# Kernel tuning notes

Hardware: AMD Instinct MI355X
Metric: run time of the kernel (lower is better)

## Reference

```python
import jax, jax.numpy as jnp
import numpy as np

N, E = 50000, 800000
DIN, DOUT = 256, 128
DH = 2 * DOUT  # hidden width of conv1


def setup_inputs() -> dict:
    key = jax.random.key(0)
    ks = jax.random.split(key, 9)
    x = jax.random.normal(ks[0], (N, DIN), dtype=jnp.float32)
    edge_index = jax.random.randint(ks[1], (2, E), 0, N, dtype=jnp.int64)
    edge_weight = jax.random.uniform(ks[2], (E,), dtype=jnp.float32)
    s1 = 1.0 / np.sqrt(DIN)
    s2 = 1.0 / np.sqrt(DH)
    W1 = jax.random.uniform(ks[3], (DIN, DH), minval=-s1, maxval=s1, dtype=jnp.float32)
    b1 = jnp.zeros((DH,), jnp.float32)
    Wmu = jax.random.uniform(ks[4], (DH, DOUT), minval=-s2, maxval=s2, dtype=jnp.float32)
    bmu = jnp.zeros((DOUT,), jnp.float32)
    Wls = jax.random.uniform(ks[5], (DH, DOUT), minval=-s2, maxval=s2, dtype=jnp.float32)
    bls = jnp.zeros((DOUT,), jnp.float32)
    return {"x": x, "edge_index": edge_index, "edge_weight": edge_weight,
            "W1": W1, "b1": b1, "Wmu": Wmu, "bmu": bmu, "Wls": Wls, "bls": bls}


def _gcn_layer(x, row, col, norm, W, b, n):
    # GCNConv: linear transform, then normalized scatter-add aggregation, then bias
    h = x @ W                                   # [N, Dout]
    msg = h[row] * norm[:, None]                # gather source feats, scale per-edge
    agg = jax.ops.segment_sum(msg, col, num_segments=n)  # scatter-add to targets
    return agg + b


def reference(x, edge_index, edge_weight, W1, b1, Wmu, bmu, Wls, bls):
    n = x.shape[0]
    row, col = edge_index[0], edge_index[1]
    # add self loops with weight 1 (PyG gcn_norm default, fill_value=1)
    loop = jnp.arange(n)
    row_f = jnp.concatenate([row, loop])
    col_f = jnp.concatenate([col, loop])
    ew = jnp.concatenate([edge_weight, jnp.ones((n,), x.dtype)])
    # symmetric normalization: deg computed over destination index
    deg = jax.ops.segment_sum(ew, col_f, num_segments=n)
    dinv = jnp.where(deg > 0, jax.lax.rsqrt(deg), 0.0)
    norm = dinv[row_f] * ew * dinv[col_f]       # cached=True -> same norm each layer
    h = jax.nn.relu(_gcn_layer(x, row_f, col_f, norm, W1, b1, n))
    mu = _gcn_layer(h, row_f, col_f, norm, Wmu, bmu, n)
    logstd = _gcn_layer(h, row_f, col_f, norm, Wls, bls, n)
    return mu, logstd
```

## Files before the change

### kernel.cpp

```cpp
#include <hip/hip_runtime.h>

#define THREADS 256

typedef __attribute__((ext_vector_type(8))) short bf16x8;
typedef __attribute__((ext_vector_type(4))) float f32x4;

#define CNT_SHIFT 20
#define DEG_SCALE 8192.0f
#define DEG_MASK  ((1u << CNT_SHIFT) - 1)

__device__ inline float bf2f(unsigned short u) {
    union { unsigned int i; float f; } v; v.i = ((unsigned int)u) << 16; return v.f;
}
__device__ inline unsigned short f2bf(float f) {
    union { float f; unsigned int i; } v; v.f = f;
    unsigned int i = v.i;
    i += 0x7fff + ((i >> 16) & 1);
    return (unsigned short)(i >> 16);
}

__global__ void k_count(const int* __restrict__ dst, const float* __restrict__ ew,
                        unsigned int* __restrict__ packed,
                        int* __restrict__ rank, int E) {
    int e = blockIdx.x * THREADS + threadIdx.x;
    if (e >= E) return;
    int c = dst[e];
    unsigned int v = (1u << CNT_SHIFT) | (unsigned int)(ew[e] * DEG_SCALE + 0.5f);
    unsigned int old = atomicAdd(&packed[c], v);
    rank[e] = (int)(old >> CNT_SHIFT);
}

__global__ void k_scan_part(const unsigned int* __restrict__ packed,
                            int* __restrict__ counts, float* __restrict__ dinv,
                            int* __restrict__ offsets, int* __restrict__ blocksum, int n) {
    __shared__ int s[THREADS];
    int i = blockIdx.x * THREADS + threadIdx.x;
    unsigned int p = (i < n) ? packed[i] : 0u;
    int v = (int)(p >> CNT_SHIFT);
    if (i < n) {
        counts[i] = v;
        float d = 1.0f + (float)(p & DEG_MASK) * (1.0f / DEG_SCALE);
        dinv[i] = rsqrtf(d);
    }
    s[threadIdx.x] = v;
    __syncthreads();
    for (int d = 1; d < THREADS; d <<= 1) {
        int t = (threadIdx.x >= d) ? s[threadIdx.x - d] : 0;
        __syncthreads();
        s[threadIdx.x] += t;
        __syncthreads();
    }
    if (i < n) offsets[i] = s[threadIdx.x] - v;
    if (threadIdx.x == THREADS - 1) blocksum[blockIdx.x] = s[THREADS - 1];
}

__global__ void k_scan_block(int* __restrict__ blocksum, int nb) {
    __shared__ int s[THREADS];
    int v = (threadIdx.x < nb) ? blocksum[threadIdx.x] : 0;
    s[threadIdx.x] = v;
    __syncthreads();
    for (int d = 1; d < THREADS; d <<= 1) {
        int t = (threadIdx.x >= d) ? s[threadIdx.x - d] : 0;
        __syncthreads();
        s[threadIdx.x] += t;
        __syncthreads();
    }
    if (threadIdx.x < nb) blocksum[threadIdx.x] = s[threadIdx.x] - v;
}

__global__ void k_scan_add(int* __restrict__ offsets, const int* __restrict__ blocksum, int n) {
    int i = blockIdx.x * THREADS + threadIdx.x;
    if (i >= n) return;
    offsets[i] += blocksum[blockIdx.x];
}

__global__ void k_fill(const int* __restrict__ ei, const float* __restrict__ ew,
                       const float* __restrict__ dinv, const int* __restrict__ offsets,
                       const int* __restrict__ rank, int2* __restrict__ epack, int E) {
    int e = blockIdx.x * THREADS + threadIdx.x;
    if (e >= E) return;
    int r = ei[e];
    int c = ei[E + e];
    int pos = offsets[c] + rank[e];
    int2 m; m.x = r; m.y = __float_as_int(dinv[r] * ew[e] * dinv[c]);
    epack[pos] = m;
}

__global__ void k_cvt_w(const float* __restrict__ W1, const float* __restrict__ Wmu,
                        const float* __restrict__ Wls, const float* __restrict__ bmu,
                        const float* __restrict__ bls,
                        ushort* __restrict__ W1t, ushort* __restrict__ Wct,
                        float* __restrict__ bcat, unsigned int* __restrict__ packed,
                        int n) {
    int nb = blockIdx.x, k = threadIdx.x;
    int gi = nb * THREADS + k;
    if (gi < n) packed[gi] = 0u;
    if (nb < 256) {
        W1t[k * 256 + nb] = f2bf(W1[nb * 256 + k]);
    } else if (nb < 512) {
        int r = nb - 256;
        float v = (k < 128) ? Wmu[r * 128 + k] : Wls[r * 128 + (k - 128)];
        Wct[k * 256 + r] = f2bf(v);
    } else {
        bcat[k] = (k < 128) ? bmu[k] : bls[k - 128];
    }
}

template<int MODE>
__global__ void k_agg(const ushort4* __restrict__ fb,
                      const int* __restrict__ eoff, const int* __restrict__ ecnt,
                      const int2* __restrict__ epack, const float* __restrict__ dinv,
                      const float* __restrict__ bias, void* __restrict__ out, int n) {
    int wave = threadIdx.x >> 6, lane = threadIdx.x & 63;
    int node = blockIdx.x * 4 + wave;
    if (node >= n) return;
    float ds = dinv[node]; ds *= ds;
    ushort4 v = fb[(size_t)node * 64 + lane];
    float ax = ds * bf2f(v.x), ay = ds * bf2f(v.y),
          az = ds * bf2f(v.z), aw = ds * bf2f(v.w);
    int e = eoff[node], cnt = ecnt[node];
    while (cnt > 0) {
        int take = cnt < 64 ? cnt : 64;
        int2 meta = make_int2(0, 0);
        if (lane < take) {
            long long m = __builtin_nontemporal_load((const long long*)&epack[e + lane]);
            meta.x = (int)m; meta.y = (int)(m >> 32);
        }
        for (int j = 0; j < take; j += 8) {
            int s0 = __builtin_amdgcn_readlane(meta.x, j + 0);
            int s1 = __builtin_amdgcn_readlane(meta.x, j + 1);
            int s2 = __builtin_amdgcn_readlane(meta.x, j + 2);
            int s3 = __builtin_amdgcn_readlane(meta.x, j + 3);
            int s4 = __builtin_amdgcn_readlane(meta.x, j + 4);
            int s5 = __builtin_amdgcn_readlane(meta.x, j + 5);
            int s6 = __builtin_amdgcn_readlane(meta.x, j + 6);
            int s7 = __builtin_amdgcn_readlane(meta.x, j + 7);
            float w0 = __int_as_float(__builtin_amdgcn_readlane(meta.y, j + 0));
            float w1 = __int_as_float(__builtin_amdgcn_readlane(meta.y, j + 1));
            float w2 = __int_as_float(__builtin_amdgcn_readlane(meta.y, j + 2));
            float w3 = __int_as_float(__builtin_amdgcn_readlane(meta.y, j + 3));
            float w4 = __int_as_float(__builtin_amdgcn_readlane(meta.y, j + 4));
            float w5 = __int_as_float(__builtin_amdgcn_readlane(meta.y, j + 5));
            float w6 = __int_as_float(__builtin_amdgcn_readlane(meta.y, j + 6));
            float w7 = __int_as_float(__builtin_amdgcn_readlane(meta.y, j + 7));
            ushort4 u0 = fb[(size_t)s0 * 64 + lane];
            ushort4 u1 = fb[(size_t)s1 * 64 + lane];
            ushort4 u2 = fb[(size_t)s2 * 64 + lane];
            ushort4 u3 = fb[(size_t)s3 * 64 + lane];
            ushort4 u4 = fb[(size_t)s4 * 64 + lane];
            ushort4 u5 = fb[(size_t)s5 * 64 + lane];
            ushort4 u6 = fb[(size_t)s6 * 64 + lane];
            ushort4 u7 = fb[(size_t)s7 * 64 + lane];
            ax += w0 * bf2f(u0.x) + w1 * bf2f(u1.x) + w2 * bf2f(u2.x) + w3 * bf2f(u3.x);
            ay += w0 * bf2f(u0.y) + w1 * bf2f(u1.y) + w2 * bf2f(u2.y) + w3 * bf2f(u3.y);
            az += w0 * bf2f(u0.z) + w1 * bf2f(u1.z) + w2 * bf2f(u2.z) + w3 * bf2f(u3.z);
            aw += w0 * bf2f(u0.w) + w1 * bf2f(u1.w) + w2 * bf2f(u2.w) + w3 * bf2f(u3.w);
            ax += w4 * bf2f(u4.x) + w5 * bf2f(u5.x) + w6 * bf2f(u6.x) + w7 * bf2f(u7.x);
            ay += w4 * bf2f(u4.y) + w5 * bf2f(u5.y) + w6 * bf2f(u6.y) + w7 * bf2f(u7.y);
            az += w4 * bf2f(u4.z) + w5 * bf2f(u5.z) + w6 * bf2f(u6.z) + w7 * bf2f(u7.z);
            aw += w4 * bf2f(u4.w) + w5 * bf2f(u5.w) + w6 * bf2f(u6.w) + w7 * bf2f(u7.w);
        }
        e += take; cnt -= take;
    }
    float4 b = ((const float4*)bias)[lane];
    ax += b.x; ay += b.y; az += b.z; aw += b.w;
    if (MODE == 0) {
        unsigned long long o =
            (unsigned long long)f2bf(fmaxf(ax, 0.f)) |
            ((unsigned long long)f2bf(fmaxf(ay, 0.f)) << 16) |
            ((unsigned long long)f2bf(fmaxf(az, 0.f)) << 32) |
            ((unsigned long long)f2bf(fmaxf(aw, 0.f)) << 48);
        __builtin_nontemporal_store(o, (unsigned long long*)out + (size_t)node * 64 + lane);
    } else {
        f32x4 o; o[0] = ax; o[1] = ay; o[2] = az; o[3] = aw;
        f32x4* mu = (f32x4*)out;
        f32x4* ls = mu + (size_t)n * 32;
        if (lane < 32) __builtin_nontemporal_store(o, &mu[(size_t)node * 32 + lane]);
        else           __builtin_nontemporal_store(o, &ls[(size_t)node * 32 + (lane - 32)]);
    }
}

#define LDT 40
template<int AF32>
__global__ __launch_bounds__(256) void k_gemm(const void* __restrict__ Ain,
        const ushort* __restrict__ Bt, ushort* __restrict__ C, int M) {
    __shared__ ushort As[128 * LDT];
    __shared__ ushort Bs[128 * LDT];
    const float*  Af = (const float*)Ain;
    const ushort* Ab = (const ushort*)Ain;
    int tid = threadIdx.x;
    int lane = tid & 63, wave = tid >> 6;
    int row0 = blockIdx.y * 128, col0 = blockIdx.x * 128;
    int mw = (wave >> 1) * 64, nw = (wave & 1) * 64;
    int lr = lane & 15, lq = lane >> 4;
    f32x4 acc[4][4] = {};
    for (int k0 = 0; k0 < 256; k0 += 32) {
        #pragma unroll
        for (int i = 0; i < 2; i++) {
            int c = tid + i * 256;
            int r = c >> 2, q = c & 3;
            int gr = row0 + r;
            int4 av = make_int4(0, 0, 0, 0);
            if (gr < M) {
                if (AF32) {
                    const float* p = Af + (size_t)gr * 256 + k0 + q * 8;
                    float4 lo = *(const float4*)p;
                    float4 hi = *(const float4*)(p + 4);
                    ushort* u = (ushort*)&av;
                    u[0] = f2bf(lo.x); u[1] = f2bf(lo.y);
                    u[2] = f2bf(lo.z); u[3] = f2bf(lo.w);
                    u[4] = f2bf(hi.x); u[5] = f2bf(hi.y);
                    u[6] = f2bf(hi.z); u[7] = f2bf(hi.w);
                } else {
                    av = *(const int4*)(Ab + (size_t)gr * 256 + k0 + q * 8);
                }
            }
            *(int4*)(&As[r * LDT + q * 8]) = av;
            int4 bv = *(const int4*)(Bt + (size_t)(col0 + r) * 256 + k0 + q * 8);
            *(int4*)(&Bs[r * LDT + q * 8]) = bv;
        }
        __syncthreads();
        bf16x8 af[4], bfr[4];
        #pragma unroll
        for (int mi = 0; mi < 4; mi++)
            af[mi] = *(const bf16x8*)(&As[(mw + mi * 16 + lr) * LDT + lq * 8]);
        #pragma unroll
        for (int ni = 0; ni < 4; ni++)
            bfr[ni] = *(const bf16x8*)(&Bs[(nw + ni * 16 + lr) * LDT + lq * 8]);
        #pragma unroll
        for (int mi = 0; mi < 4; mi++)
            #pragma unroll
            for (int ni = 0; ni < 4; ni++)
                acc[mi][ni] = __builtin_amdgcn_mfma_f32_16x16x32_bf16(
                    af[mi], bfr[ni], acc[mi][ni], 0, 0, 0);
        __syncthreads();
    }
    #pragma unroll
    for (int mi = 0; mi < 4; mi++)
        #pragma unroll
        for (int ni = 0; ni < 4; ni++)
            #pragma unroll
            for (int r = 0; r < 4; r++) {
                int grow = row0 + mw + mi * 16 + lq * 4 + r;
                int gcol = col0 + nw + ni * 16 + lr;
                if (grow < M) C[(size_t)grow * 256 + gcol] = f2bf(acc[mi][ni][r]);
            }
}

extern "C" void kernel_launch(void* const* d_in, const int* in_sizes, int n_in,
                              void* d_out, int out_size, void* d_ws, size_t ws_size,
                              hipStream_t stream) {
    const float* x   = (const float*)d_in[0];
    const int*   ei  = (const int*)d_in[1];
    const float* ew  = (const float*)d_in[2];
    const float* W1  = (const float*)d_in[3];
    const float* b1  = (const float*)d_in[4];
    const float* Wmu = (const float*)d_in[5];
    const float* bmu = (const float*)d_in[6];
    const float* Wls = (const float*)d_in[7];
    const float* bls = (const float*)d_in[8];

    const int DIN = 256;
    const int N = in_sizes[0] / DIN;
    const int E = in_sizes[2];

    unsigned int* packed = (unsigned int*)d_ws;
    int*   counts   = (int*)(packed + N);
    int*   offsets  = counts + N;
    float* dinv     = (float*)(offsets + N);
    int*   blocksum = (int*)(dinv + N);
    int*   rank     = blocksum + 256;
    int2*  epack    = (int2*)(rank + E);
    ushort* xw      = (ushort*)(epack + E);
    ushort* hb      = xw + (size_t)N * 256;
    ushort* hw      = hb + (size_t)N * 256;
    ushort* W1t     = hw + (size_t)N * 256;
    ushort* Wct     = W1t + 256 * 256;
    float*  bcat    = (float*)(Wct + 256 * 256);

    int gN = (N + THREADS - 1) / THREADS;
    int gE = (E + THREADS - 1) / THREADS;

    k_cvt_w<<<513, THREADS, 0, stream>>>(W1, Wmu, Wls, bmu, bls, W1t, Wct, bcat,
                                         packed, N);
    k_count<<<gE, THREADS, 0, stream>>>(ei + E, ew, packed, rank, E);

    k_scan_part<<<gN, THREADS, 0, stream>>>(packed, counts, dinv, offsets, blocksum, N);
    k_scan_block<<<1, THREADS, 0, stream>>>(blocksum, gN);
    k_scan_add<<<gN, THREADS, 0, stream>>>(offsets, blocksum, N);

    k_fill<<<gE, THREADS, 0, stream>>>(ei, ew, dinv, offsets, rank, epack, E);

    int gAgg = (N + 3) / 4;
    dim3 ggrid(2, (N + 127) / 128);

    k_gemm<1><<<ggrid, 256, 0, stream>>>(x, W1t, xw, N);
    k_agg<0><<<gAgg, THREADS, 0, stream>>>((const ushort4*)xw, offsets, counts,
                                           epack, dinv, b1, hb, N);

    k_gemm<0><<<ggrid, 256, 0, stream>>>(hb, Wct, hw, N);
    k_agg<1><<<gAgg, THREADS, 0, stream>>>((const ushort4*)hw, offsets, counts,
                                           epack, dinv, bcat, d_out, N);
}
```

Before: 358.0 us.

## Widen GEMM tile to full output width, fold scan-add into consumers, nontemporal loads

The GEMM now uses 512-thread blocks, each covering all 256 output columns for a 128-row tile. The A tile (including the fp32-to-bf16 conversion of x) is therefore loaded and converted once per row block instead of twice. The separate scan-add kernel is removed, and the block prefix sums are added on the fly in k_fill and k_agg, saving one launch and one pass over the offsets array. Streaming loads and stores in the count, fill and GEMM kernels are marked nontemporal to reduce cache pollution. In exchange, the larger GEMM tile doubles LDS use for B and may lower occupancy.

```diff
diff --git a/kernel.cpp b/kernel.cpp
--- a/kernel.cpp
+++ b/kernel.cpp
@@ -4,6 +4,7 @@
 
 typedef __attribute__((ext_vector_type(8))) short bf16x8;
 typedef __attribute__((ext_vector_type(4))) float f32x4;
+typedef __attribute__((ext_vector_type(4))) int i32x4;
 
 #define CNT_SHIFT 20
 #define DEG_SCALE 8192.0f
@@ -24,10 +25,11 @@
                         int* __restrict__ rank, int E) {
     int e = blockIdx.x * THREADS + threadIdx.x;
     if (e >= E) return;
-    int c = dst[e];
-    unsigned int v = (1u << CNT_SHIFT) | (unsigned int)(ew[e] * DEG_SCALE + 0.5f);
+    int c = __builtin_nontemporal_load(dst + e);
+    float w = __builtin_nontemporal_load(ew + e);
+    unsigned int v = (1u << CNT_SHIFT) | (unsigned int)(w * DEG_SCALE + 0.5f);
     unsigned int old = atomicAdd(&packed[c], v);
-    rank[e] = (int)(old >> CNT_SHIFT);
+    __builtin_nontemporal_store((int)(old >> CNT_SHIFT), rank + e);
 }
 
 __global__ void k_scan_part(const unsigned int* __restrict__ packed,
@@ -68,22 +70,20 @@
     if (threadIdx.x < nb) blocksum[threadIdx.x] = s[threadIdx.x] - v;
 }
 
-__global__ void k_scan_add(int* __restrict__ offsets, const int* __restrict__ blocksum, int n) {
-    int i = blockIdx.x * THREADS + threadIdx.x;
-    if (i >= n) return;
-    offsets[i] += blocksum[blockIdx.x];
-}
-
 __global__ void k_fill(const int* __restrict__ ei, const float* __restrict__ ew,
                        const float* __restrict__ dinv, const int* __restrict__ offsets,
+                       const int* __restrict__ bsum,
                        const int* __restrict__ rank, int2* __restrict__ epack, int E) {
     int e = blockIdx.x * THREADS + threadIdx.x;
     if (e >= E) return;
-    int r = ei[e];
-    int c = ei[E + e];
-    int pos = offsets[c] + rank[e];
-    int2 m; m.x = r; m.y = __float_as_int(dinv[r] * ew[e] * dinv[c]);
-    epack[pos] = m;
+    int r = __builtin_nontemporal_load(ei + e);
+    int c = __builtin_nontemporal_load(ei + E + e);
+    float w = __builtin_nontemporal_load(ew + e);
+    int rk = __builtin_nontemporal_load(rank + e);
+    int pos = offsets[c] + bsum[c >> 8] + rk;
+    long long m = (long long)r |
+        ((long long)__float_as_int(dinv[r] * w * dinv[c]) << 32);
+    __builtin_nontemporal_store(m, (long long*)&epack[pos]);
 }
 
 __global__ void k_cvt_w(const float* __restrict__ W1, const float* __restrict__ Wmu,
@@ -109,6 +109,7 @@
 template<int MODE>
 __global__ void k_agg(const ushort4* __restrict__ fb,
                       const int* __restrict__ eoff, const int* __restrict__ ecnt,
+                      const int* __restrict__ bsum,
                       const int2* __restrict__ epack, const float* __restrict__ dinv,
                       const float* __restrict__ bias, void* __restrict__ out, int n) {
     int wave = threadIdx.x >> 6, lane = threadIdx.x & 63;
@@ -118,7 +119,7 @@
     ushort4 v = fb[(size_t)node * 64 + lane];
     float ax = ds * bf2f(v.x), ay = ds * bf2f(v.y),
           az = ds * bf2f(v.z), aw = ds * bf2f(v.w);
-    int e = eoff[node], cnt = ecnt[node];
+    int e = eoff[node] + bsum[node >> 8], cnt = ecnt[node];
     while (cnt > 0) {
         int take = cnt < 64 ? cnt : 64;
         int2 meta = make_int2(0, 0);
@@ -182,42 +183,46 @@
 
 #define LDT 40
 template<int AF32>
-__global__ __launch_bounds__(256) void k_gemm(const void* __restrict__ Ain,
+__global__ __launch_bounds__(512) void k_gemm(const void* __restrict__ Ain,
         const ushort* __restrict__ Bt, ushort* __restrict__ C, int M) {
     __shared__ ushort As[128 * LDT];
-    __shared__ ushort Bs[128 * LDT];
+    __shared__ ushort Bs[256 * LDT];
     const float*  Af = (const float*)Ain;
     const ushort* Ab = (const ushort*)Ain;
     int tid = threadIdx.x;
     int lane = tid & 63, wave = tid >> 6;
-    int row0 = blockIdx.y * 128, col0 = blockIdx.x * 128;
-    int mw = (wave >> 1) * 64, nw = (wave & 1) * 64;
+    int row0 = blockIdx.x * 128;
+    int mw = (wave >> 2) * 64, nw = (wave & 3) * 64;
     int lr = lane & 15, lq = lane >> 4;
     f32x4 acc[4][4] = {};
     for (int k0 = 0; k0 < 256; k0 += 32) {
-        #pragma unroll
-        for (int i = 0; i < 2; i++) {
-            int c = tid + i * 256;
-            int r = c >> 2, q = c & 3;
+        {
+            int r = tid >> 2, q = tid & 3;
             int gr = row0 + r;
-            int4 av = make_int4(0, 0, 0, 0);
+            i32x4 av = {0, 0, 0, 0};
             if (gr < M) {
                 if (AF32) {
                     const float* p = Af + (size_t)gr * 256 + k0 + q * 8;
-                    float4 lo = *(const float4*)p;
-                    float4 hi = *(const float4*)(p + 4);
+                    i32x4 lo = __builtin_nontemporal_load((const i32x4*)p);
+                    i32x4 hi = __builtin_nontemporal_load((const i32x4*)(p + 4));
                     ushort* u = (ushort*)&av;
-                    u[0] = f2bf(lo.x); u[1] = f2bf(lo.y);
-                    u[2] = f2bf(lo.z); u[3] = f2bf(lo.w);
-                    u[4] = f2bf(hi.x); u[5] = f2bf(hi.y);
-                    u[6] = f2bf(hi.z); u[7] = f2bf(hi.w);
+                    u[0] = f2bf(__int_as_float(lo[0])); u[1] = f2bf(__int_as_float(lo[1]));
+                    u[2] = f2bf(__int_as_float(lo[2])); u[3] = f2bf(__int_as_float(lo[3]));
+                    u[4] = f2bf(__int_as_float(hi[0])); u[5] = f2bf(__int_as_float(hi[1]));
+                    u[6] = f2bf(__int_as_float(hi[2])); u[7] = f2bf(__int_as_float(hi[3]));
                 } else {
-                    av = *(const int4*)(Ab + (size_t)gr * 256 + k0 + q * 8);
+                    av = __builtin_nontemporal_load(
+                        (const i32x4*)(Ab + (size_t)gr * 256 + k0 + q * 8));
                 }
             }
-            *(int4*)(&As[r * LDT + q * 8]) = av;
-            int4 bv = *(const int4*)(Bt + (size_t)(col0 + r) * 256 + k0 + q * 8);
-            *(int4*)(&Bs[r * LDT + q * 8]) = bv;
+            *(i32x4*)(&As[r * LDT + q * 8]) = av;
+        }
+        #pragma unroll
+        for (int i = 0; i < 2; i++) {
+            int c = tid + i * 512;
+            int r = c >> 2, q = c & 3;
+            i32x4 bv = *(const i32x4*)(Bt + (size_t)r * 256 + k0 + q * 8);
+            *(i32x4*)(&Bs[r * LDT + q * 8]) = bv;
         }
         __syncthreads();
         bf16x8 af[4], bfr[4];
@@ -242,7 +247,7 @@
             #pragma unroll
             for (int r = 0; r < 4; r++) {
                 int grow = row0 + mw + mi * 16 + lq * 4 + r;
-                int gcol = col0 + nw + ni * 16 + lr;
+                int gcol = nw + ni * 16 + lr;
                 if (grow < M) C[(size_t)grow * 256 + gcol] = f2bf(acc[mi][ni][r]);
             }
 }
@@ -287,18 +292,17 @@
 
     k_scan_part<<<gN, THREADS, 0, stream>>>(packed, counts, dinv, offsets, blocksum, N);
     k_scan_block<<<1, THREADS, 0, stream>>>(blocksum, gN);
-    k_scan_add<<<gN, THREADS, 0, stream>>>(offsets, blocksum, N);
-
-    k_fill<<<gE, THREADS, 0, stream>>>(ei, ew, dinv, offsets, rank, epack, E);
+
+    k_fill<<<gE, THREADS, 0, stream>>>(ei, ew, dinv, offsets, blocksum, rank, epack, E);
 
     int gAgg = (N + 3) / 4;
-    dim3 ggrid(2, (N + 127) / 128);
-
-    k_gemm<1><<<ggrid, 256, 0, stream>>>(x, W1t, xw, N);
+    int gG = (N + 127) / 128;
+
+    k_gemm<1><<<gG, 512, 0, stream>>>(x, W1t, xw, N);
     k_agg<0><<<gAgg, THREADS, 0, stream>>>((const ushort4*)xw, offsets, counts,
-                                           epack, dinv, b1, hb, N);
-
-    k_gemm<0><<<ggrid, 256, 0, stream>>>(hb, Wct, hw, N);
+                                           blocksum, epack, dinv, b1, hb, N);
+
+    k_gemm<0><<<gG, 512, 0, stream>>>(hb, Wct, hw, N);
     k_agg<1><<<gAgg, THREADS, 0, stream>>>((const ushort4*)hw, offsets, counts,
-                                           epack, dinv, bcat, d_out, N);
-}
+                                           blocksum, epack, dinv, bcat, d_out, N);
+}
```

New measurement: 333.3 us. 1.07x faster.
